# Performance work log

Hardware: AMD Instinct MI355X
Metric: run time of the kernel (lower is better)

## Reference

```python
import jax, jax.numpy as jnp
import numpy as np

NUM_BEV_FEATURES = 64
NX, NY, NZ = 512, 512, 1
P_PER_BATCH = 30000
BATCH = 4


def setup_inputs() -> dict:
    key = jax.random.key(0)
    pillar_features = jax.random.normal(key, (BATCH * P_PER_BATCH, NUM_BEV_FEATURES), dtype=jnp.float32)
    # Build coords (batch, z, y, x) with unique (y, x) cells per batch (realistic voxelization)
    rng = np.random.default_rng(0)
    coords_list = []
    for b in range(BATCH):
        flat = rng.choice(NY * NX, size=P_PER_BATCH, replace=False)
        y = flat // NX
        x = flat % NX
        c = np.stack([np.full(P_PER_BATCH, b), np.zeros(P_PER_BATCH, dtype=np.int64), y, x], axis=1)
        coords_list.append(c)
    coords = jnp.asarray(np.concatenate(coords_list, axis=0), dtype=jnp.int64)
    return {"pillar_features": pillar_features, "coords": coords, "batch_size": BATCH}


def reference(pillar_features, coords, batch_size):
    # Fused single-scatter equivalent of the per-batch loop in PointPillarScatter.
    # Per-batch cell index: z + y*nx + x; add batch offset to scatter all at once.
    cell = coords[:, 1] + coords[:, 2] * NX + coords[:, 3]          # [P]
    flat_idx = coords[:, 0] * (NZ * NY * NX) + cell                  # [P]
    grid = jnp.zeros((batch_size * NZ * NY * NX, NUM_BEV_FEATURES), dtype=pillar_features.dtype)
    grid = grid.at[flat_idx].set(pillar_features)                    # [B*ny*nx, C]
    # channels_first output: [B, C*nz, ny, nx]
    out = grid.reshape(batch_size, NY, NX, NUM_BEV_FEATURES)
    return jnp.transpose(out, (0, 3, 1, 2))
```

## Files before the change

### kernel.cpp

```cpp
#include <hip/hip_runtime.h>

#define GNX 512
#define GNY 512
#define GC  64

typedef float vfloat4 __attribute__((ext_vector_type(4)));
typedef int   vint4   __attribute__((ext_vector_type(4)));

__global__ void pp_fill_map(vint4* __restrict__ map, int n4) {
    int i = blockIdx.x * blockDim.x + threadIdx.x;
    if (i < n4) {
        vint4 m1 = { -1, -1, -1, -1 };
        map[i] = m1;
    }
}

__global__ void pp_scatter_idx(const vint4* __restrict__ coords,
                               int* __restrict__ map, int P) {
    int p = blockIdx.x * blockDim.x + threadIdx.x;
    if (p >= P) return;
    vint4 c = coords[p];
    map[c[0] * (GNY * GNX) + c[1] + c[2] * GNX + c[3]] = p;
}

__global__ void __launch_bounds__(256) pp_gather_out(
        const float* __restrict__ feat, const int* __restrict__ map,
        float* __restrict__ out, int nquad) {
    int q  = blockIdx.x * blockDim.x + threadIdx.x;
    if (q >= nquad) return;
    int cg = blockIdx.y;

    int x4 = q & (GNX / 4 - 1);
    int y  = (q >> 7) & (GNY - 1);
    int b  = q >> 16;

    int cellbase = (b << 18) + (y << 9) + (x4 << 2);
    vint4 m = *(const vint4*)(map + cellbase);

    vfloat4 fr[4][2];
#pragma unroll
    for (int j = 0; j < 4; ++j) {
        fr[j][0] = (vfloat4)0.f;
        fr[j][1] = (vfloat4)0.f;
    }

#pragma unroll
    for (int j = 0; j < 4; ++j) {
        int pj = m[j];
        if (pj >= 0) {
            const vfloat4* fp = (const vfloat4*)(feat + (pj << 6) + (cg << 3));
            fr[j][0] = fp[0];
            fr[j][1] = fp[1];
        }
    }

    int rowoff = (y << 9) + (x4 << 2);
    float* obase = out + (((b << 6) + (cg << 3)) << 18) + rowoff;
#pragma unroll
    for (int k = 0; k < 2; ++k) {
#pragma unroll
        for (int t = 0; t < 4; ++t) {
            vfloat4 v = { fr[0][k][t], fr[1][k][t], fr[2][k][t], fr[3][k][t] };
            *(vfloat4*)(obase + ((k * 4 + t) << 18)) = v;
        }
    }
}

extern "C" void kernel_launch(void* const* d_in, const int* in_sizes, int n_in,
                              void* d_out, int out_size, void* d_ws, size_t ws_size,
                              hipStream_t stream) {
    const float* feat   = (const float*)d_in[0];
    const int*   coords = (const int*)d_in[1];
    int P = in_sizes[1] / 4;
    int B = out_size / (GC * GNY * GNX);
    int* map = (int*)d_ws;
    int mapN = B * GNY * GNX;

    int n4 = mapN / 4;
    pp_fill_map<<<(n4 + 255) / 256, 256, 0, stream>>>((vint4*)map, n4);
    pp_scatter_idx<<<(P + 255) / 256, 256, 0, stream>>>(
        (const vint4*)coords, map, P);

    int nquad = B * GNY * (GNX / 4);
    dim3 grid((nquad + 255) / 256, GC / 8, 1);
    pp_gather_out<<<grid, 256, 0, stream>>>(feat, map, (float*)d_out, nquad);
}
```

Before: 301.2 us.

## Use persistent grid-stride gather with map prefetch and nontemporal output stores

```diff
diff --git a/kernel.cpp b/kernel.cpp
--- a/kernel.cpp
+++ b/kernel.cpp
@@ -25,44 +25,63 @@
 
 __global__ void __launch_bounds__(256) pp_gather_out(
         const float* __restrict__ feat, const int* __restrict__ map,
-        float* __restrict__ out, int nquad) {
-    int q  = blockIdx.x * blockDim.x + threadIdx.x;
-    if (q >= nquad) return;
-    int cg = blockIdx.y;
+        float* __restrict__ out, int nwork, int nqlog) {
+    int idx    = blockIdx.x * blockDim.x + threadIdx.x;
+    int stride = gridDim.x * blockDim.x;
+    if (idx >= nwork) return;
 
-    int x4 = q & (GNX / 4 - 1);
-    int y  = (q >> 7) & (GNY - 1);
-    int b  = q >> 16;
+    int qmask = (1 << nqlog) - 1;
 
-    int cellbase = (b << 18) + (y << 9) + (x4 << 2);
-    vint4 m = *(const vint4*)(map + cellbase);
+    int w  = idx;
+    int qq = w & qmask;
+    int x4 = qq & (GNX / 4 - 1);
+    int y  = (qq >> 7) & (GNY - 1);
+    int b  = qq >> 16;
+    vint4 m = *(const vint4*)(map + (b << 18) + (y << 9) + (x4 << 2));
 
-    vfloat4 fr[4][2];
+    while (true) {
+        int wn = w + stride;
+        bool more = wn < nwork;
+        vint4 mn = { -1, -1, -1, -1 };
+        int x4n = 0, yn = 0, bn = 0;
+        if (more) {
+            int qn = wn & qmask;
+            x4n = qn & (GNX / 4 - 1);
+            yn  = (qn >> 7) & (GNY - 1);
+            bn  = qn >> 16;
+            mn = *(const vint4*)(map + (bn << 18) + (yn << 9) + (x4n << 2));
+        }
+
+        int cg = w >> nqlog;
+        vfloat4 fr[4][2];
 #pragma unroll
-    for (int j = 0; j < 4; ++j) {
-        fr[j][0] = (vfloat4)0.f;
-        fr[j][1] = (vfloat4)0.f;
-    }
+        for (int j = 0; j < 4; ++j) {
+            fr[j][0] = (vfloat4)0.f;
+            fr[j][1] = (vfloat4)0.f;
+        }
+#pragma unroll
+        for (int j = 0; j < 4; ++j) {
+            int pj = m[j];
+            if (pj >= 0) {
+                const vfloat4* fp = (const vfloat4*)(feat + (pj << 6) + (cg << 3));
+                fr[j][0] = fp[0];
+                fr[j][1] = fp[1];
+            }
+        }
 
+        int rowoff = (y << 9) + (x4 << 2);
+        float* obase = out + (((b << 6) + (cg << 3)) << 18) + rowoff;
 #pragma unroll
-    for (int j = 0; j < 4; ++j) {
-        int pj = m[j];
-        if (pj >= 0) {
-            const vfloat4* fp = (const vfloat4*)(feat + (pj << 6) + (cg << 3));
-            fr[j][0] = fp[0];
-            fr[j][1] = fp[1];
+        for (int k = 0; k < 2; ++k) {
+#pragma unroll
+            for (int t = 0; t < 4; ++t) {
+                vfloat4 v = { fr[0][k][t], fr[1][k][t], fr[2][k][t], fr[3][k][t] };
+                __builtin_nontemporal_store(v, (vfloat4*)(obase + ((k * 4 + t) << 18)));
+            }
         }
-    }
 
-    int rowoff = (y << 9) + (x4 << 2);
-    float* obase = out + (((b << 6) + (cg << 3)) << 18) + rowoff;
-#pragma unroll
-    for (int k = 0; k < 2; ++k) {
-#pragma unroll
-        for (int t = 0; t < 4; ++t) {
-            vfloat4 v = { fr[0][k][t], fr[1][k][t], fr[2][k][t], fr[3][k][t] };
-            *(vfloat4*)(obase + ((k * 4 + t) << 18)) = v;
-        }
+        if (!more) break;
+        w = wn; m = mn; x4 = x4n; y = yn; b = bn;
     }
 }
 
@@ -82,6 +101,8 @@
         (const vint4*)coords, map, P);
 
     int nquad = B * GNY * (GNX / 4);
-    dim3 grid((nquad + 255) / 256, GC / 8, 1);
-    pp_gather_out<<<grid, 256, 0, stream>>>(feat, map, (float*)d_out, nquad);
+    int nwork = nquad * (GC / 8);
+    int nqlog = 31 - __builtin_clz((unsigned)nquad);
+    pp_gather_out<<<2048, 256, 0, stream>>>(feat, map, (float*)d_out,
+                                            nwork, nqlog);
 }
```

Measured after the change: 293.8 us. -2.5%, faster.

## Process all channels per thread with double-buffered loads, zero-row pointers, nontemporal stores

Applied to the files above, without the earlier changes.

```diff
diff --git a/kernel.cpp b/kernel.cpp
--- a/kernel.cpp
+++ b/kernel.cpp
@@ -13,6 +13,10 @@
         vint4 m1 = { -1, -1, -1, -1 };
         map[i] = m1;
     }
+    if (i < 16) {
+        vint4 z = { 0, 0, 0, 0 };
+        map[n4 + i] = z;
+    }
 }
 
 __global__ void pp_scatter_idx(const vint4* __restrict__ coords,
@@ -23,46 +27,56 @@
     map[c[0] * (GNY * GNX) + c[1] + c[2] * GNX + c[3]] = p;
 }
 
+#define LOADCG(fr, cg) do {                                            \
+    int off_ = ((cg) << 3);                                            \
+    _Pragma("unroll")                                                  \
+    for (int j = 0; j < 4; ++j) {                                      \
+        const vfloat4* fp_ = (const vfloat4*)(bj[j] + off_);           \
+        fr[j][0] = fp_[0];                                             \
+        fr[j][1] = fp_[1];                                             \
+    }                                                                  \
+} while (0)
+
+#define STORECG(fr, cg) do {                                           \
+    float* ob_ = obase + (((cg) << 3) << 18);                          \
+    _Pragma("unroll")                                                  \
+    for (int k = 0; k < 2; ++k)                                        \
+    _Pragma("unroll")                                                  \
+    for (int t = 0; t < 4; ++t) {                                      \
+        vfloat4 v_ = { fr[0][k][t], fr[1][k][t], fr[2][k][t], fr[3][k][t] }; \
+        __builtin_nontemporal_store(v_, (vfloat4*)(ob_ + (((k << 2) + t) << 18))); \
+    }                                                                  \
+} while (0)
+
 __global__ void __launch_bounds__(256) pp_gather_out(
         const float* __restrict__ feat, const int* __restrict__ map,
-        float* __restrict__ out, int nquad) {
-    int q  = blockIdx.x * blockDim.x + threadIdx.x;
+        const float* __restrict__ zrow, float* __restrict__ out, int nquad) {
+    int q = blockIdx.x * blockDim.x + threadIdx.x;
     if (q >= nquad) return;
-    int cg = blockIdx.y;
 
     int x4 = q & (GNX / 4 - 1);
     int y  = (q >> 7) & (GNY - 1);
     int b  = q >> 16;
 
-    int cellbase = (b << 18) + (y << 9) + (x4 << 2);
-    vint4 m = *(const vint4*)(map + cellbase);
+    vint4 m = *(const vint4*)(map + (b << 18) + (y << 9) + (x4 << 2));
 
-    vfloat4 fr[4][2];
-#pragma unroll
-    for (int j = 0; j < 4; ++j) {
-        fr[j][0] = (vfloat4)0.f;
-        fr[j][1] = (vfloat4)0.f;
-    }
-
+    const float* bj[4];
 #pragma unroll
     for (int j = 0; j < 4; ++j) {
         int pj = m[j];
-        if (pj >= 0) {
-            const vfloat4* fp = (const vfloat4*)(feat + (pj << 6) + (cg << 3));
-            fr[j][0] = fp[0];
-            fr[j][1] = fp[1];
-        }
+        bj[j] = (pj >= 0) ? (feat + (pj << 6)) : zrow;
     }
 
-    int rowoff = (y << 9) + (x4 << 2);
-    float* obase = out + (((b << 6) + (cg << 3)) << 18) + rowoff;
+    float* obase = out + (((b << 6)) << 18) + (y << 9) + (x4 << 2);
+
+    vfloat4 frA[4][2], frB[4][2];
+    LOADCG(frA, 0);
 #pragma unroll
-    for (int k = 0; k < 2; ++k) {
-#pragma unroll
-        for (int t = 0; t < 4; ++t) {
-            vfloat4 v = { fr[0][k][t], fr[1][k][t], fr[2][k][t], fr[3][k][t] };
-            *(vfloat4*)(obase + ((k * 4 + t) << 18)) = v;
-        }
+    for (int c2 = 0; c2 < 4; ++c2) {
+        LOADCG(frB, 2 * c2 + 1);
+        STORECG(frA, 2 * c2);
+        if (c2 < 3) LOADCG(frA, 2 * c2 + 2);
+        STORECG(frB, 2 * c2 + 1);
     }
 }
 
@@ -75,6 +89,7 @@
     int B = out_size / (GC * GNY * GNX);
     int* map = (int*)d_ws;
     int mapN = B * GNY * GNX;
+    const float* zrow = (const float*)(map + mapN);
 
     int n4 = mapN / 4;
     pp_fill_map<<<(n4 + 255) / 256, 256, 0, stream>>>((vint4*)map, n4);
@@ -82,6 +97,6 @@
         (const vint4*)coords, map, P);
 
     int nquad = B * GNY * (GNX / 4);
-    dim3 grid((nquad + 255) / 256, GC / 8, 1);
-    pp_gather_out<<<grid, 256, 0, stream>>>(feat, map, (float*)d_out, nquad);
+    pp_gather_out<<<(nquad + 255) / 256, 256, 0, stream>>>(
+        feat, map, zrow, (float*)d_out, nquad);
 }
```

Result: no change. 295.4 us (-1.9%).
